# Performance work log

Measured on AMD Instinct MI355X. Metric: run time of the kernel, lower is better.

Reference implementation:

```python
import jax, jax.numpy as jnp
import numpy as np

N_NODES = 50000
N_EDGES = 800000
N_GRAPHS = 256
IN_CH = 128
HID = 128
OUT_CH = 10
BN_EPS = 1e-5


def setup_inputs() -> dict:
    key = jax.random.key(0)
    ks = jax.random.split(key, 32)
    x = jax.random.normal(ks[0], (N_NODES, IN_CH), dtype=jnp.float32)
    edge_index = jax.random.randint(ks[1], (2, N_EDGES), 0, N_NODES)
    batch = jnp.sort(jax.random.randint(ks[2], (N_NODES,), 0, N_GRAPHS))

    def lin(k, fan_in, fan_out):
        return (jax.random.normal(k, (fan_in, fan_out), dtype=jnp.float32)
                * np.float32(1.0 / np.sqrt(fan_in)))

    inp = {"x": x, "edge_index": edge_index, "batch": batch}
    dims = [(IN_CH, HID), (HID, HID), (HID, HID)]
    for i, (fi, fo) in enumerate(dims):
        inp[f"W{i}"] = lin(ks[3 + i], fi, fo)
        inp[f"b{i}"] = jnp.zeros((fo,), jnp.float32)
        inp[f"g{i}"] = jnp.ones((fo,), jnp.float32)
        inp[f"be{i}"] = jnp.zeros((fo,), jnp.float32)
    inp["lin1_w"] = lin(ks[10], 2 * HID, HID)
    inp["lin1_b"] = jnp.zeros((HID,), jnp.float32)
    inp["lin2_w"] = lin(ks[11], HID, OUT_CH)
    inp["lin2_b"] = jnp.zeros((OUT_CH,), jnp.float32)
    return inp


def _gcn_conv(x, W, b, src, dst):
    # PyG GCNConv: h = X W; add self-loops; symmetric D^-1/2 (A+I) D^-1/2 aggregation.
    h = x @ W  # [N, F]
    loops = jnp.arange(N_NODES)
    s = jnp.concatenate([src, loops])
    d = jnp.concatenate([dst, loops])
    deg = jax.ops.segment_sum(jnp.ones_like(d, jnp.float32), d, num_segments=N_NODES)
    dinv = jnp.where(deg > 0, jax.lax.rsqrt(deg), 0.0)
    coef = dinv[s] * dinv[d]  # [E+N]
    out = jax.ops.segment_sum(h[s] * coef[:, None], d, num_segments=N_NODES)
    return out + b


def _batch_norm(x, gamma, beta):
    mean = x.mean(axis=0)
    var = x.var(axis=0)
    return (x - mean) * jax.lax.rsqrt(var + BN_EPS) * gamma + beta


def _forward(x, edge_index, batch,
             W0, b0, g0, be0, W1, b1, g1, be1, W2, b2, g2, be2,
             lin1_w, lin1_b, lin2_w, lin2_b):
    src, dst = edge_index[0], edge_index[1]
    for W, b, g, be in ((W0, b0, g0, be0), (W1, b1, g1, be1), (W2, b2, g2, be2)):
        x = _gcn_conv(x, W, b, src, dst)
        x = jax.nn.relu(_batch_norm(x, g, be))
    x_sum = jax.ops.segment_sum(x, batch, num_segments=N_GRAPHS)  # [G, H]
    counts = jax.ops.segment_sum(jnp.ones((N_NODES,), jnp.float32), batch,
                                 num_segments=N_GRAPHS)
    x_mean = x_sum / jnp.maximum(counts, 1.0)[:, None]
    h = jnp.concatenate([x_mean, x_sum], axis=1)  # [G, 2H]
    h = jax.nn.relu(h @ lin1_w + lin1_b)
    return h @ lin2_w + lin2_b  # [G, OUT_CH]


def reference(x, edge_index, batch,
              W0, b0, g0, be0, W1, b1, g1, be1, W2, b2, g2, be2,
              lin1_w, lin1_b, lin2_w, lin2_b):
    return _forward(x, edge_index, batch,
                    W0, b0, g0, be0, W1, b1, g1, be1, W2, b2, g2, be2,
                    lin1_w, lin1_b, lin2_w, lin2_b)
```

## Files before the change

### kernel.cpp

```cpp
#include <hip/hip_runtime.h>

#define N_NODES 50000
#define N_EDGES 800000
#define N_GRAPHS 256
#define HID 128
#define OUT_CH 10
#define BN_EPS 1e-5f

#define NBUCKET 98
#define BCAP 10240

#define OFF_H       0
#define OFF_BNPART  3134464
#define OFF_CSRD    3200000
#define OFF_WBT     4000000
#define OFF_AGG     6400000
#define OFF_ROWPTR  12850000
#define OFF_CSR     12950004
#define OFF_DINV    13750004
#define OFF_BNCOEF  13800004
#define OFF_POOL    13800260
#define OFF_CNT     13833028
#define OFF_BCNT    13833284
#define OFF_BSTART  13833444

#define WBT_PITCH 136

typedef __attribute__((ext_vector_type(8))) short bf16x8;
typedef __attribute__((ext_vector_type(4))) float f32x4;

__device__ __forceinline__ ushort f2bf(float f) {
    union { float f; unsigned u; } v; v.f = f;
    unsigned r = v.u + 0x7FFFu + ((v.u >> 16) & 1u);
    return (ushort)(r >> 16);
}
__device__ __forceinline__ float bf2f(unsigned u16) {
    return __uint_as_float(u16 << 16);
}

__global__ void k_zero(int* bcnt) {
    int i = threadIdx.x;
    if (i < NBUCKET) bcnt[i] = 0;
}

__global__ __launch_bounds__(256) void k_bucket(const int* __restrict__ ei,
                                                int* __restrict__ bcnt,
                                                int2* __restrict__ buf) {
    __shared__ int histL[NBUCKET], baseL[NBUCKET], curL[NBUCKET];
    int t = threadIdx.x;
    if (t < NBUCKET) histL[t] = 0;
    __syncthreads();
    const int stride = gridDim.x * 256;
    for (int i = blockIdx.x * 256 + t; i < N_EDGES; i += stride)
        atomicAdd(&histL[ei[N_EDGES + i] >> 9], 1);
    __syncthreads();
    if (t < NBUCKET) {
        baseL[t] = atomicAdd(&bcnt[t], histL[t]);
        curL[t] = 0;
    }
    __syncthreads();
    for (int i = blockIdx.x * 256 + t; i < N_EDGES; i += stride) {
        int s = ei[i];
        int d = ei[N_EDGES + i];
        int b = d >> 9;
        int p = baseL[b] + atomicAdd(&curL[b], 1);
        if (p < BCAP) buf[b * BCAP + p] = make_int2(s, d);
    }
}

__global__ void k_bscan(const int* __restrict__ bcnt, int* __restrict__ bstart,
                        int* __restrict__ rowptr) {
    if (threadIdx.x == 0) {
        int acc = 0;
        for (int b = 0; b < NBUCKET; ++b) { bstart[b] = acc; acc += bcnt[b]; }
        bstart[NBUCKET] = acc;
        rowptr[N_NODES] = acc;
    }
}

__global__ __launch_bounds__(512) void k_csrbuild(const int2* __restrict__ buf,
                                                  const int* __restrict__ bcnt,
                                                  const int* __restrict__ bstart,
                                                  int* __restrict__ rowptr,
                                                  int* __restrict__ csr,
                                                  float* __restrict__ dinv) {
    __shared__ int off[512];
    __shared__ int cur[512];
    int b = blockIdx.x, t = threadIdx.x;
    int node0 = b << 9;
    int cnt = bcnt[b];
    int ebase = bstart[b];
    const int2* mybuf = buf + b * BCAP;

    off[t] = 0;
    __syncthreads();
    for (int e = t; e < cnt; e += 512)
        atomicAdd(&off[mybuf[e].y - node0], 1);
    __syncthreads();
    int mydeg = off[t];
    for (int o = 1; o < 512; o <<= 1) {
        int x = (t >= o) ? off[t - o] : 0;
        __syncthreads();
        off[t] += x;
        __syncthreads();
    }
    int inc = off[t];
    cur[t] = ebase + inc - mydeg;
    int node = node0 + t;
    if (node < N_NODES) {
        rowptr[node] = ebase + inc - mydeg;
        dinv[node] = rsqrtf((float)(mydeg + 1));
    }
    __syncthreads();
    for (int e = t; e < cnt; e += 512) {
        int2 pr = mybuf[e];
        int p = atomicAdd(&cur[pr.y - node0], 1);
        csr[p] = pr.x;
    }
}

__global__ __launch_bounds__(256) void k_sortseg(const int* __restrict__ rowptr,
                                                 int* __restrict__ csr,
                                                 const float* __restrict__ dinv,
                                                 float* __restrict__ csrd) {
    int wave = threadIdx.x >> 6, lane = threadIdx.x & 63;
    int v = blockIdx.x * 4 + wave;
    if (v >= N_NODES) return;
    int e0 = rowptr[v], deg = rowptr[v + 1] - e0;
    if (deg <= 64) {
        int val = (lane < deg) ? csr[e0 + lane] : 0x7FFFFFFF;
#pragma unroll
        for (int k = 2; k <= 64; k <<= 1)
#pragma unroll
            for (int j = k >> 1; j > 0; j >>= 1) {
                int other = __shfl_xor(val, j);
                bool up = ((lane & k) == 0);
                bool lower = ((lane & j) == 0);
                int mn = min(val, other), mx = max(val, other);
                val = (up == lower) ? mn : mx;
            }
        if (lane < deg) {
            csr[e0 + lane] = val;
            csrd[e0 + lane] = dinv[val];
        }
    } else {
        if (lane == 0) {
            for (int i = e0 + 1; i < e0 + deg; ++i) {
                int key = csr[i];
                int j = i - 1;
                while (j >= e0 && csr[j] > key) { csr[j + 1] = csr[j]; --j; }
                csr[j + 1] = key;
            }
        }
        for (int e = e0 + lane; e < e0 + deg; e += 64) csrd[e] = dinv[csr[e]];
    }
}

__global__ void k_wprep(const float* __restrict__ W, ushort* __restrict__ Wbt) {
    int i = blockIdx.x * 256 + threadIdx.x;
    if (i < 16384) {
        int k = i >> 7, c = i & 127;
        Wbt[c * WBT_PITCH + k] = f2bf(W[i]);
    }
}

template <int BN>
__global__ __launch_bounds__(256) void k_gemm(const float* __restrict__ X,
                                              const ushort* __restrict__ Wbt,
                                              ushort* __restrict__ Hb,
                                              const float* __restrict__ coef,
                                              int nrows) {
    __shared__ __align__(16) ushort Wt[128 * WBT_PITCH];
    int t = threadIdx.x;
    for (int i = t; i < 2176; i += 256)
        ((uint4*)Wt)[i] = ((const uint4*)Wbt)[i];
    __syncthreads();

    int wv = t >> 6, l = t & 63;
    int m = l & 15;
    int kg = l >> 4;
    int row = blockIdx.x * 64 + wv * 16 + m;
    bool valid = row < nrows;
    const float* xr = X + (long)row * 128;

    f32x4 acc[8];
#pragma unroll
    for (int n = 0; n < 8; ++n) acc[n] = (f32x4){0.f, 0.f, 0.f, 0.f};

#pragma unroll
    for (int t4 = 0; t4 < 4; ++t4) {
        int k0 = t4 * 32 + kg * 8;
        float xv[8];
        if (valid) {
            float4 u0 = *(const float4*)(xr + k0);
            float4 u1 = *(const float4*)(xr + k0 + 4);
            if (BN) {
                float4 s0 = *(const float4*)(coef + k0);
                float4 s1 = *(const float4*)(coef + k0 + 4);
                float4 h0 = *(const float4*)(coef + 128 + k0);
                float4 h1 = *(const float4*)(coef + 128 + k0 + 4);
                u0.x = fmaxf(u0.x * s0.x + h0.x, 0.f);
                u0.y = fmaxf(u0.y * s0.y + h0.y, 0.f);
                u0.z = fmaxf(u0.z * s0.z + h0.z, 0.f);
                u0.w = fmaxf(u0.w * s0.w + h0.w, 0.f);
                u1.x = fmaxf(u1.x * s1.x + h1.x, 0.f);
                u1.y = fmaxf(u1.y * s1.y + h1.y, 0.f);
                u1.z = fmaxf(u1.z * s1.z + h1.z, 0.f);
                u1.w = fmaxf(u1.w * s1.w + h1.w, 0.f);
            }
            xv[0] = u0.x; xv[1] = u0.y; xv[2] = u0.z; xv[3] = u0.w;
            xv[4] = u1.x; xv[5] = u1.y; xv[6] = u1.z; xv[7] = u1.w;
        } else {
#pragma unroll
            for (int j = 0; j < 8; ++j) xv[j] = 0.f;
        }
        union { ushort u[8]; bf16x8 v; } A;
#pragma unroll
        for (int j = 0; j < 8; ++j) A.u[j] = f2bf(xv[j]);

#pragma unroll
        for (int n = 0; n < 8; ++n) {
            bf16x8 b = *(const bf16x8*)(&Wt[(n * 16 + m) * WBT_PITCH + k0]);
            acc[n] = __builtin_amdgcn_mfma_f32_16x16x32_bf16(A.v, b, acc[n], 0, 0, 0);
        }
    }

    int srow0 = blockIdx.x * 64 + wv * 16 + kg * 4;
#pragma unroll
    for (int n = 0; n < 8; ++n)
#pragma unroll
        for (int r = 0; r < 4; ++r) {
            int rr = srow0 + r;
            if (rr < nrows) Hb[(long)rr * 128 + n * 16 + m] = f2bf(acc[n][r]);
        }
}

__global__ __launch_bounds__(256) void k_agg(const ushort* __restrict__ Hb,
                                             const int* __restrict__ rowptr,
                                             const int* __restrict__ csr,
                                             const float* __restrict__ csrd,
                                             const float* __restrict__ dinv,
                                             const float* __restrict__ bias,
                                             float* __restrict__ OUT) {
    int wave = threadIdx.x >> 6, lane = threadIdx.x & 63;
    int v = blockIdx.x * 4 + wave;
    if (v >= N_NODES) return;
    int half = lane >> 5, qd = lane & 31;
    int c = qd * 4;
    float dv = dinv[v];
    int e0 = rowptr[v];
    int deg = rowptr[v + 1] - e0;
    float a0 = 0.f, a1 = 0.f, a2 = 0.f, a3 = 0.f;

    for (int base = 0; base < deg; base += 64) {
        int mye = base + lane;
        int idx = 0; float dvi = 0.f;
        if (mye < deg) { idx = csr[e0 + mye]; dvi = csrd[e0 + mye]; }
        int n = min(64, deg - base);
        int P = (n + 1) >> 1;
        int p = 0;
#define EDGE(pp) { \
        int sl = 2 * (pp) + half; \
        int s = __shfl(idx, sl); \
        float cf = __shfl(dvi, sl) * dv; \
        uint2 qv = *(const uint2*)(Hb + (long)s * 128 + c); \
        a0 += cf * bf2f(qv.x & 0xFFFFu); \
        a1 += cf * bf2f(qv.x >> 16); \
        a2 += cf * bf2f(qv.y & 0xFFFFu); \
        a3 += cf * bf2f(qv.y >> 16); }
        for (; p + 4 <= P; p += 4) { EDGE(p) EDGE(p + 1) EDGE(p + 2) EDGE(p + 3) }
        for (; p < P; ++p) { EDGE(p) }
#undef EDGE
    }
    a0 += __shfl_xor(a0, 32);
    a1 += __shfl_xor(a1, 32);
    a2 += __shfl_xor(a2, 32);
    a3 += __shfl_xor(a3, 32);
    if (half == 0) {
        uint2 qv = *(const uint2*)(Hb + (long)v * 128 + c);
        float cs = dv * dv;
        float4 bb = *(const float4*)(bias + c);
        float4 o;
        o.x = a0 + cs * bf2f(qv.x & 0xFFFFu) + bb.x;
        o.y = a1 + cs * bf2f(qv.x >> 16) + bb.y;
        o.z = a2 + cs * bf2f(qv.y & 0xFFFFu) + bb.z;
        o.w = a3 + cs * bf2f(qv.y >> 16) + bb.w;
        *(float4*)(OUT + (long)v * 128 + c) = o;
    }
}

__global__ __launch_bounds__(256) void k_bnstats(const float* __restrict__ X,
                                                 float* __restrict__ part) {
    int ch = threadIdx.x & 127;
    int half = threadIdx.x >> 7;
    float s = 0.f, q = 0.f;
    for (int v = blockIdx.x * 2 + half; v < N_NODES; v += 512) {
        float x = X[(long)v * 128 + ch];
        s += x;
        q += x * x;
    }
    __shared__ float sh[256];
    sh[threadIdx.x] = s;
    __syncthreads();
    float s2 = (half == 0) ? s + sh[threadIdx.x + 128] : 0.f;
    __syncthreads();
    sh[threadIdx.x] = q;
    __syncthreads();
    if (half == 0) {
        float q2 = q + sh[threadIdx.x + 128];
        part[blockIdx.x * 256 + ch] = s2;
        part[blockIdx.x * 256 + 128 + ch] = q2;
    }
}

__global__ void k_bnred(const float* __restrict__ part, const float* __restrict__ g,
                        const float* __restrict__ be, float* __restrict__ coef) {
    int t = threadIdx.x;
    int ch = t & 127, stat = t >> 7;
    float acc = 0.f;
    for (int b = 0; b < 256; ++b) acc += part[b * 256 + stat * 128 + ch];
    __shared__ float sh[256];
    sh[t] = acc;
    __syncthreads();
    if (stat == 0) {
        float inv_n = 1.0f / (float)N_NODES;
        float mean = acc * inv_n;
        float var = sh[128 + ch] * inv_n - mean * mean;
        float sc = g[ch] * rsqrtf(var + BN_EPS);
        coef[ch] = sc;
        coef[128 + ch] = be[ch] - mean * sc;
    }
}

__global__ __launch_bounds__(256) void k_pool(const float* __restrict__ X,
                                              const int* __restrict__ batch,
                                              const float* __restrict__ coef,
                                              float* __restrict__ pool,
                                              float* __restrict__ cnt) {
    __shared__ int bounds[2];
    int g = blockIdx.x, t = threadIdx.x;
    if (t < 2) {
        int target = g + t;
        int lo = 0, hi = N_NODES;
        while (lo < hi) {
            int mid = (lo + hi) >> 1;
            if (batch[mid] < target) lo = mid + 1; else hi = mid;
        }
        bounds[t] = lo;
    }
    __syncthreads();
    int start = bounds[0], end = bounds[1];
    int ch = t & 127, half = t >> 7;
    float sc = coef[ch], sh = coef[128 + ch];
    float acc = 0.f;
    for (int v = start + half; v < end; v += 2)
        acc += fmaxf(X[(long)v * 128 + ch] * sc + sh, 0.f);
    __shared__ float red[256];
    red[t] = acc;
    __syncthreads();
    if (half == 0) {
        pool[g * 128 + ch] = red[ch] + red[128 + ch];
        if (ch == 0) cnt[g] = (float)(end - start);
    }
}

__global__ __launch_bounds__(128) void k_mlp(const float* __restrict__ pool,
                                             const float* __restrict__ cnt,
                                             const float* __restrict__ w1,
                                             const float* __restrict__ b1,
                                             const float* __restrict__ w2,
                                             const float* __restrict__ b2,
                                             float* __restrict__ out) {
    __shared__ float h[256];
    __shared__ float h1[128];
    int g = blockIdx.x, t = threadIdx.x;
    float s = pool[g * 128 + t];
    float c = cnt[g];
    h[t] = s / fmaxf(c, 1.0f);
    h[128 + t] = s;
    __syncthreads();
    float acc = b1[t];
#pragma unroll 4
    for (int i = 0; i < 256; ++i) acc += h[i] * w1[i * 128 + t];
    h1[t] = fmaxf(acc, 0.f);
    __syncthreads();
    if (t < OUT_CH) {
        float o = b2[t];
#pragma unroll 4
        for (int j = 0; j < 128; ++j) o += h1[j] * w2[j * OUT_CH + t];
        out[g * OUT_CH + t] = o;
    }
}

extern "C" void kernel_launch(void* const* d_in, const int* in_sizes, int n_in,
                              void* d_out, int out_size, void* d_ws, size_t ws_size,
                              hipStream_t stream) {
    const float* x = (const float*)d_in[0];
    const int* ei = (const int*)d_in[1];
    const int* batch = (const int*)d_in[2];
    const float* W[3] = {(const float*)d_in[3], (const float*)d_in[7], (const float*)d_in[11]};
    const float* b[3] = {(const float*)d_in[4], (const float*)d_in[8], (const float*)d_in[12]};
    const float* gm[3] = {(const float*)d_in[5], (const float*)d_in[9], (const float*)d_in[13]};
    const float* be[3] = {(const float*)d_in[6], (const float*)d_in[10], (const float*)d_in[14]};
    const float* w1 = (const float*)d_in[15];
    const float* b1 = (const float*)d_in[16];
    const float* w2 = (const float*)d_in[17];
    const float* b2 = (const float*)d_in[18];
    float* out = (float*)d_out;

    float* ws = (float*)d_ws;
    ushort* Hb = (ushort*)(ws + OFF_H);
    float* bnpart = ws + OFF_BNPART;
    float* csrd = ws + OFF_CSRD;
    ushort* Wbt = (ushort*)(ws + OFF_WBT);
    float* AGG = ws + OFF_AGG;
    int2* bucketBuf = (int2*)(ws + OFF_AGG);
    int* rowptr = (int*)(ws + OFF_ROWPTR);
    int* csr = (int*)(ws + OFF_CSR);
    float* dinv = ws + OFF_DINV;
    float* bncoef = ws + OFF_BNCOEF;
    float* pool = ws + OFF_POOL;
    float* cnt = ws + OFF_CNT;
    int* bcnt = (int*)(ws + OFF_BCNT);
    int* bstart = (int*)(ws + OFF_BSTART);

    const int nb_node4 = (N_NODES + 3) / 4;

    hipLaunchKernelGGL(k_zero, dim3(1), dim3(128), 0, stream, bcnt);
    hipLaunchKernelGGL(k_bucket, dim3(392), dim3(256), 0, stream, ei, bcnt, bucketBuf);
    hipLaunchKernelGGL(k_bscan, dim3(1), dim3(64), 0, stream, bcnt, bstart, rowptr);
    hipLaunchKernelGGL(k_csrbuild, dim3(NBUCKET), dim3(512), 0, stream,
                       bucketBuf, bcnt, bstart, rowptr, csr, dinv);
    hipLaunchKernelGGL(k_sortseg, dim3(nb_node4), dim3(256), 0, stream,
                       rowptr, csr, dinv, csrd);
    for (int layer = 0; layer < 3; ++layer)
        hipLaunchKernelGGL(k_wprep, dim3(64), dim3(256), 0, stream,
                           W[layer], Wbt + layer * 128 * WBT_PITCH);

    const int gemm_blocks = (N_NODES + 63) / 64;
    for (int layer = 0; layer < 3; ++layer) {
        const float* cur_x = (layer == 0) ? x : AGG;
        const ushort* wbt_l = Wbt + layer * 128 * WBT_PITCH;
        if (layer == 0) {
            hipLaunchKernelGGL(k_gemm<0>, dim3(gemm_blocks), dim3(256), 0, stream,
                               cur_x, wbt_l, Hb, (const float*)nullptr, N_NODES);
        } else {
            hipLaunchKernelGGL(k_gemm<1>, dim3(gemm_blocks), dim3(256), 0, stream,
                               cur_x, wbt_l, Hb, bncoef, N_NODES);
        }
        hipLaunchKernelGGL(k_agg, dim3(nb_node4), dim3(256), 0, stream,
                           Hb, rowptr, csr, csrd, dinv, b[layer], AGG);
        hipLaunchKernelGGL(k_bnstats, dim3(256), dim3(256), 0, stream, AGG, bnpart);
        hipLaunchKernelGGL(k_bnred, dim3(1), dim3(256), 0, stream,
                           bnpart, gm[layer], be[layer], bncoef);
    }

    hipLaunchKernelGGL(k_pool, dim3(N_GRAPHS), dim3(256), 0, stream,
                       AGG, batch, bncoef, pool, cnt);
    hipLaunchKernelGGL(k_mlp, dim3(N_GRAPHS), dim3(128), 0, stream,
                       pool, cnt, w1, b1, w2, b2, out);
}
```

Baseline: 449.1 us.

## Fuse small launches and widen aggregation loads to 16-byte rows

```diff
diff --git a/kernel.cpp b/kernel.cpp
--- a/kernel.cpp
+++ b/kernel.cpp
@@ -19,10 +19,8 @@
 #define OFF_CSR     12950004
 #define OFF_DINV    13750004
 #define OFF_BNCOEF  13800004
-#define OFF_POOL    13800260
 #define OFF_CNT     13833028
 #define OFF_BCNT    13833284
-#define OFF_BSTART  13833444
 
 #define WBT_PITCH 136
 
@@ -68,32 +66,28 @@
     }
 }
 
-__global__ void k_bscan(const int* __restrict__ bcnt, int* __restrict__ bstart,
-                        int* __restrict__ rowptr) {
-    if (threadIdx.x == 0) {
-        int acc = 0;
-        for (int b = 0; b < NBUCKET; ++b) { bstart[b] = acc; acc += bcnt[b]; }
-        bstart[NBUCKET] = acc;
-        rowptr[N_NODES] = acc;
-    }
-}
-
 __global__ __launch_bounds__(512) void k_csrbuild(const int2* __restrict__ buf,
                                                   const int* __restrict__ bcnt,
-                                                  const int* __restrict__ bstart,
                                                   int* __restrict__ rowptr,
                                                   int* __restrict__ csr,
                                                   float* __restrict__ dinv) {
     __shared__ int off[512];
     __shared__ int cur[512];
+    __shared__ int ebase_s;
     int b = blockIdx.x, t = threadIdx.x;
     int node0 = b << 9;
     int cnt = bcnt[b];
-    int ebase = bstart[b];
     const int2* mybuf = buf + b * BCAP;
 
+    if (t == 0) {
+        int acc = 0;
+        for (int i = 0; i < b; ++i) acc += bcnt[i];
+        ebase_s = acc;
+        if (b == NBUCKET - 1) rowptr[N_NODES] = acc + cnt;
+    }
     off[t] = 0;
     __syncthreads();
+    int ebase = ebase_s;
     for (int e = t; e < cnt; e += 512)
         atomicAdd(&off[mybuf[e].y - node0], 1);
     __syncthreads();
@@ -156,11 +150,14 @@
     }
 }
 
-__global__ void k_wprep(const float* __restrict__ W, ushort* __restrict__ Wbt) {
+__global__ void k_wprep3(const float* __restrict__ W0, const float* __restrict__ W1,
+                         const float* __restrict__ W2, ushort* __restrict__ Wbt) {
     int i = blockIdx.x * 256 + threadIdx.x;
-    if (i < 16384) {
-        int k = i >> 7, c = i & 127;
-        Wbt[c * WBT_PITCH + k] = f2bf(W[i]);
+    if (i < 3 * 16384) {
+        int layer = i / 16384, r = i - layer * 16384;
+        const float* W = (layer == 0) ? W0 : (layer == 1) ? W1 : W2;
+        int k = r >> 7, c = r & 127;
+        Wbt[layer * 128 * WBT_PITCH + c * WBT_PITCH + k] = f2bf(W[r]);
     }
 }
 
@@ -245,47 +242,62 @@
     int wave = threadIdx.x >> 6, lane = threadIdx.x & 63;
     int v = blockIdx.x * 4 + wave;
     if (v >= N_NODES) return;
-    int half = lane >> 5, qd = lane & 31;
-    int c = qd * 4;
+    int q = lane >> 4, ql = lane & 15;
+    int c = ql * 8;
     float dv = dinv[v];
     int e0 = rowptr[v];
     int deg = rowptr[v + 1] - e0;
     float a0 = 0.f, a1 = 0.f, a2 = 0.f, a3 = 0.f;
+    float a4 = 0.f, a5 = 0.f, a6 = 0.f, a7 = 0.f;
 
     for (int base = 0; base < deg; base += 64) {
         int mye = base + lane;
         int idx = 0; float dvi = 0.f;
         if (mye < deg) { idx = csr[e0 + mye]; dvi = csrd[e0 + mye]; }
         int n = min(64, deg - base);
-        int P = (n + 1) >> 1;
+        int P = (n + 3) >> 2;
         int p = 0;
 #define EDGE(pp) { \
-        int sl = 2 * (pp) + half; \
+        int sl = 4 * (pp) + q; \
         int s = __shfl(idx, sl); \
         float cf = __shfl(dvi, sl) * dv; \
-        uint2 qv = *(const uint2*)(Hb + (long)s * 128 + c); \
+        uint4 qv = *(const uint4*)(Hb + (long)s * 128 + c); \
         a0 += cf * bf2f(qv.x & 0xFFFFu); \
         a1 += cf * bf2f(qv.x >> 16); \
         a2 += cf * bf2f(qv.y & 0xFFFFu); \
-        a3 += cf * bf2f(qv.y >> 16); }
+        a3 += cf * bf2f(qv.y >> 16); \
+        a4 += cf * bf2f(qv.z & 0xFFFFu); \
+        a5 += cf * bf2f(qv.z >> 16); \
+        a6 += cf * bf2f(qv.w & 0xFFFFu); \
+        a7 += cf * bf2f(qv.w >> 16); }
         for (; p + 4 <= P; p += 4) { EDGE(p) EDGE(p + 1) EDGE(p + 2) EDGE(p + 3) }
         for (; p < P; ++p) { EDGE(p) }
 #undef EDGE
     }
-    a0 += __shfl_xor(a0, 32);
-    a1 += __shfl_xor(a1, 32);
-    a2 += __shfl_xor(a2, 32);
-    a3 += __shfl_xor(a3, 32);
-    if (half == 0) {
-        uint2 qv = *(const uint2*)(Hb + (long)v * 128 + c);
+    a0 += __shfl_xor(a0, 16); a0 += __shfl_xor(a0, 32);
+    a1 += __shfl_xor(a1, 16); a1 += __shfl_xor(a1, 32);
+    a2 += __shfl_xor(a2, 16); a2 += __shfl_xor(a2, 32);
+    a3 += __shfl_xor(a3, 16); a3 += __shfl_xor(a3, 32);
+    a4 += __shfl_xor(a4, 16); a4 += __shfl_xor(a4, 32);
+    a5 += __shfl_xor(a5, 16); a5 += __shfl_xor(a5, 32);
+    a6 += __shfl_xor(a6, 16); a6 += __shfl_xor(a6, 32);
+    a7 += __shfl_xor(a7, 16); a7 += __shfl_xor(a7, 32);
+    if (q == 0) {
+        uint4 qv = *(const uint4*)(Hb + (long)v * 128 + c);
         float cs = dv * dv;
-        float4 bb = *(const float4*)(bias + c);
-        float4 o;
-        o.x = a0 + cs * bf2f(qv.x & 0xFFFFu) + bb.x;
-        o.y = a1 + cs * bf2f(qv.x >> 16) + bb.y;
-        o.z = a2 + cs * bf2f(qv.y & 0xFFFFu) + bb.z;
-        o.w = a3 + cs * bf2f(qv.y >> 16) + bb.w;
-        *(float4*)(OUT + (long)v * 128 + c) = o;
+        float4 b0 = *(const float4*)(bias + c);
+        float4 b1 = *(const float4*)(bias + c + 4);
+        float4 o0, o1;
+        o0.x = a0 + cs * bf2f(qv.x & 0xFFFFu) + b0.x;
+        o0.y = a1 + cs * bf2f(qv.x >> 16) + b0.y;
+        o0.z = a2 + cs * bf2f(qv.y & 0xFFFFu) + b0.z;
+        o0.w = a3 + cs * bf2f(qv.y >> 16) + b0.w;
+        o1.x = a4 + cs * bf2f(qv.z & 0xFFFFu) + b1.x;
+        o1.y = a5 + cs * bf2f(qv.z >> 16) + b1.y;
+        o1.z = a6 + cs * bf2f(qv.w & 0xFFFFu) + b1.z;
+        o1.w = a7 + cs * bf2f(qv.w >> 16) + b1.w;
+        *(float4*)(OUT + (long)v * 128 + c) = o0;
+        *(float4*)(OUT + (long)v * 128 + c + 4) = o1;
     }
 }
 
@@ -332,12 +344,18 @@
     }
 }
 
-__global__ __launch_bounds__(256) void k_pool(const float* __restrict__ X,
-                                              const int* __restrict__ batch,
-                                              const float* __restrict__ coef,
-                                              float* __restrict__ pool,
-                                              float* __restrict__ cnt) {
+__global__ __launch_bounds__(256) void k_poolmlp(const float* __restrict__ X,
+                                                 const int* __restrict__ batch,
+                                                 const float* __restrict__ coef,
+                                                 const float* __restrict__ w1,
+                                                 const float* __restrict__ b1,
+                                                 const float* __restrict__ w2,
+                                                 const float* __restrict__ b2,
+                                                 float* __restrict__ out) {
     __shared__ int bounds[2];
+    __shared__ float red[256];
+    __shared__ float h[256];
+    __shared__ float h1[128];
     int g = blockIdx.x, t = threadIdx.x;
     if (t < 2) {
         int target = g + t;
@@ -351,38 +369,24 @@
     __syncthreads();
     int start = bounds[0], end = bounds[1];
     int ch = t & 127, half = t >> 7;
-    float sc = coef[ch], sh = coef[128 + ch];
+    float sc = coef[ch], shv = coef[128 + ch];
     float acc = 0.f;
     for (int v = start + half; v < end; v += 2)
-        acc += fmaxf(X[(long)v * 128 + ch] * sc + sh, 0.f);
-    __shared__ float red[256];
+        acc += fmaxf(X[(long)v * 128 + ch] * sc + shv, 0.f);
     red[t] = acc;
     __syncthreads();
     if (half == 0) {
-        pool[g * 128 + ch] = red[ch] + red[128 + ch];
-        if (ch == 0) cnt[g] = (float)(end - start);
-    }
-}
-
-__global__ __launch_bounds__(128) void k_mlp(const float* __restrict__ pool,
-                                             const float* __restrict__ cnt,
-                                             const float* __restrict__ w1,
-                                             const float* __restrict__ b1,
-                                             const float* __restrict__ w2,
-                                             const float* __restrict__ b2,
-                                             float* __restrict__ out) {
-    __shared__ float h[256];
-    __shared__ float h1[128];
-    int g = blockIdx.x, t = threadIdx.x;
-    float s = pool[g * 128 + t];
-    float c = cnt[g];
-    h[t] = s / fmaxf(c, 1.0f);
-    h[128 + t] = s;
-    __syncthreads();
-    float acc = b1[t];
+        float s = red[ch] + red[128 + ch];
+        h[128 + ch] = s;
+        h[ch] = s / fmaxf((float)(end - start), 1.0f);
+    }
+    __syncthreads();
+    if (t < 128) {
+        float a = b1[t];
 #pragma unroll 4
-    for (int i = 0; i < 256; ++i) acc += h[i] * w1[i * 128 + t];
-    h1[t] = fmaxf(acc, 0.f);
+        for (int i = 0; i < 256; ++i) a += h[i] * w1[i * 128 + t];
+        h1[t] = fmaxf(a, 0.f);
+    }
     __syncthreads();
     if (t < OUT_CH) {
         float o = b2[t];
@@ -419,23 +423,18 @@
     int* csr = (int*)(ws + OFF_CSR);
     float* dinv = ws + OFF_DINV;
     float* bncoef = ws + OFF_BNCOEF;
-    float* pool = ws + OFF_POOL;
-    float* cnt = ws + OFF_CNT;
     int* bcnt = (int*)(ws + OFF_BCNT);
-    int* bstart = (int*)(ws + OFF_BSTART);
 
     const int nb_node4 = (N_NODES + 3) / 4;
 
     hipLaunchKernelGGL(k_zero, dim3(1), dim3(128), 0, stream, bcnt);
     hipLaunchKernelGGL(k_bucket, dim3(392), dim3(256), 0, stream, ei, bcnt, bucketBuf);
-    hipLaunchKernelGGL(k_bscan, dim3(1), dim3(64), 0, stream, bcnt, bstart, rowptr);
     hipLaunchKernelGGL(k_csrbuild, dim3(NBUCKET), dim3(512), 0, stream,
-                       bucketBuf, bcnt, bstart, rowptr, csr, dinv);
+                       bucketBuf, bcnt, rowptr, csr, dinv);
     hipLaunchKernelGGL(k_sortseg, dim3(nb_node4), dim3(256), 0, stream,
                        rowptr, csr, dinv, csrd);
-    for (int layer = 0; layer < 3; ++layer)
-        hipLaunchKernelGGL(k_wprep, dim3(64), dim3(256), 0, stream,
-                           W[layer], Wbt + layer * 128 * WBT_PITCH);
+    hipLaunchKernelGGL(k_wprep3, dim3(192), dim3(256), 0, stream,
+                       W[0], W[1], W[2], Wbt);
 
     const int gemm_blocks = (N_NODES + 63) / 64;
     for (int layer = 0; layer < 3; ++layer) {
@@ -455,8 +454,6 @@
                            bnpart, gm[layer], be[layer], bncoef);
     }
 
-    hipLaunchKernelGGL(k_pool, dim3(N_GRAPHS), dim3(256), 0, stream,
-                       AGG, batch, bncoef, pool, cnt);
-    hipLaunchKernelGGL(k_mlp, dim3(N_GRAPHS), dim3(128), 0, stream,
-                       pool, cnt, w1, b1, w2, b2, out);
-}
+    hipLaunchKernelGGL(k_poolmlp, dim3(N_GRAPHS), dim3(256), 0, stream,
+                       AGG, batch, bncoef, w1, b1, w2, b2, out);
+}
```

New measurement: 429.1 us. -4.4%, faster.
